# Kernel tuning notes

Measured on AMD Instinct MI355X. Metric: run time of the kernel, lower is better.

Reference implementation:

```python
import jax, jax.numpy as jnp
import numpy as np

D = 512
H = 8
DH = D // H
EPS = 1e-5


def layer_norm(x, gamma, beta):
    mu = jnp.mean(x, axis=-1, keepdims=True)
    var = jnp.mean(jnp.square(x - mu), axis=-1, keepdims=True)
    return (x - mu) * jax.lax.rsqrt(var + EPS) * gamma + beta


def setup_inputs() -> dict:
    key = jax.random.key(0)
    ks = jax.random.split(key, 16)
    B, N = 16, 1024
    s = 1.0 / np.sqrt(D)
    return {
        "h": jax.random.normal(ks[0], (B, N, D), jnp.float32),
        "ln1_g": jnp.ones((D,), jnp.float32),
        "ln1_b": jnp.zeros((D,), jnp.float32),
        "wq": jax.random.normal(ks[1], (D, D), jnp.float32) * s,
        "bq": jnp.zeros((D,), jnp.float32),
        "wk": jax.random.normal(ks[2], (D, D), jnp.float32) * s,
        "bk": jnp.zeros((D,), jnp.float32),
        "wv": jax.random.normal(ks[3], (D, D), jnp.float32) * s,
        "bv": jnp.zeros((D,), jnp.float32),
        "wo": jax.random.normal(ks[4], (D, D), jnp.float32) * s,
        "bo": jnp.zeros((D,), jnp.float32),
        "ln2_g": jnp.ones((D,), jnp.float32),
        "ln2_b": jnp.zeros((D,), jnp.float32),
        "w1": jax.random.normal(ks[5], (2 * D, D), jnp.float32) * s,
        "b1": jnp.zeros((2 * D,), jnp.float32),
        "w2": jax.random.normal(ks[6], (D, 2 * D), jnp.float32) * (1.0 / np.sqrt(2 * D)),
        "b2": jnp.zeros((D,), jnp.float32),
    }


def reference(h, ln1_g, ln1_b, wq, bq, wk, bk, wv, bv, wo, bo,
              ln2_g, ln2_b, w1, b1, w2, b2):
    B, N, _ = h.shape
    hn = layer_norm(h, ln1_g, ln1_b)
    # projections (torch Linear convention: x @ W^T + b)
    q = (hn @ wq.T + bq).reshape(B, N, H, DH)
    k = (hn @ wk.T + bk).reshape(B, N, H, DH)
    v = (hn @ wv.T + bv).reshape(B, N, H, DH)
    scores = jnp.einsum("bqhd,bkhd->bhqk", q, k) / np.sqrt(DH)
    attn = jax.nn.softmax(scores, axis=-1)  # [B,H,N,N]
    ctx = jnp.einsum("bhqk,bkhd->bqhd", attn, v).reshape(B, N, D)
    attn_out = ctx @ wo.T + bo
    # averaged attention weights (torch default average_attn_weights=True)
    attn_weights = jnp.mean(attn, axis=1)  # [B,N,N]
    h = h + attn_out
    # FFN: LN -> Linear(d,2d) -> SiLU -> Linear(2d,d), residual
    f = layer_norm(h, ln2_g, ln2_b)
    f = jax.nn.silu(f @ w1.T + b1) @ w2.T + b2
    h = h + f
    return h, attn_weights
```

## Files before the change

### kernel.cpp

```cpp
#include <hip/hip_runtime.h>

typedef unsigned short u16;
typedef __attribute__((ext_vector_type(8))) short short8;
typedef __attribute__((ext_vector_type(4))) float floatx4;
typedef __attribute__((ext_vector_type(16))) float floatx16;

#define MFMA_BF16(a, b, c) __builtin_amdgcn_mfma_f32_16x16x32_bf16((a), (b), (c), 0, 0, 0)
#define MFMA32(a, b, c) __builtin_amdgcn_mfma_f32_32x32x16_bf16((a), (b), (c), 0, 0, 0)

__device__ __forceinline__ u16 f2bf(float f) {
  unsigned b = __float_as_uint(f);
  b = b + 0x7FFFu + ((b >> 16) & 1u);
  return (u16)(b >> 16);
}

__device__ __forceinline__ float fexp8(float s) {
  float r;
  asm("v_exp_f32 %0, %1" : "=v"(r) : "v"(s * 0.18033688011112042f));
  return r;
}

__device__ __forceinline__ unsigned cvtpk(float a, float b) {
  unsigned r;
  asm("v_cvt_pk_bf16_f32 %0, %1, %2" : "=v"(r) : "v"(a), "v"(b));
  return r;
}

__device__ __forceinline__ void plswap(unsigned& x, unsigned& y) {
  asm("v_permlane32_swap_b32 %0, %1" : "+v"(x), "+v"(y));
}

__device__ __forceinline__ void gll16(const u16* g, u16* lds_uniform) {
  __builtin_amdgcn_global_load_lds(
      (const __attribute__((address_space(1))) void*)g,
      (__attribute__((address_space(3))) void*)lds_uniform, 16, 0, 0);
}

__global__ __launch_bounds__(256) void cast4_kernel(const float* __restrict__ src,
                                                    u16* __restrict__ dst, int n4) {
  int i = blockIdx.x * 256 + threadIdx.x;
  if (i < n4) {
    float4 v = ((const float4*)src)[i];
    ushort4 o;
    o.x = f2bf(v.x); o.y = f2bf(v.y); o.z = f2bf(v.z); o.w = f2bf(v.w);
    ((ushort4*)dst)[i] = o;
  }
}

__global__ __launch_bounds__(128) void ln_kernel(const float* __restrict__ x,
                                                 const float* __restrict__ g,
                                                 const float* __restrict__ be,
                                                 u16* __restrict__ y) {
  int row = blockIdx.x, t = threadIdx.x;
  float4 v = ((const float4*)(x + (size_t)row * 512))[t];
  float s = v.x + v.y + v.z + v.w;
  float q = v.x * v.x + v.y * v.y + v.z * v.z + v.w * v.w;
#pragma unroll
  for (int off = 32; off > 0; off >>= 1) {
    s += __shfl_xor(s, off);
    q += __shfl_xor(q, off);
  }
  __shared__ float sb[2], qb[2];
  int w = t >> 6;
  if ((t & 63) == 0) { sb[w] = s; qb[w] = q; }
  __syncthreads();
  s = sb[0] + sb[1];
  q = qb[0] + qb[1];
  float mu = s * (1.0f / 512.0f);
  float var = q * (1.0f / 512.0f) - mu * mu;
  float rs = rsqrtf(var + 1e-5f);
  float4 gg = ((const float4*)g)[t];
  float4 bb = ((const float4*)be)[t];
  ushort4 o;
  o.x = f2bf((v.x - mu) * rs * gg.x + bb.x);
  o.y = f2bf((v.y - mu) * rs * gg.y + bb.y);
  o.z = f2bf((v.z - mu) * rs * gg.z + bb.z);
  o.w = f2bf((v.w - mu) * rs * gg.w + bb.w);
  ((ushort4*)(y + (size_t)row * 512))[t] = o;
}

template <bool OUTB, bool SILU, bool RES>
__global__ __launch_bounds__(256) void gemm_bt_kernel(
    const u16* __restrict__ A, const u16* __restrict__ W,
    const float* __restrict__ bias, const float* __restrict__ res,
    void* __restrict__ out, int N, int K) {
  __shared__ __align__(16) u16 As[128 * 32];
  __shared__ __align__(16) u16 Bs[128 * 32];
  int t = threadIdx.x;
  int lane = t & 63, wave = t >> 6;
  int l15 = lane & 15, quad = lane >> 4;
  int rowBlk = blockIdx.y * 128, colBlk = blockIdx.x * 128;
  const u16* Ag = A + (size_t)(rowBlk + (t >> 2)) * K + (t & 3) * 8;
  const u16* Wg = W + (size_t)(colBlk + (t >> 2)) * K + (t & 3) * 8;
  u16* AsW = As + wave * 512;
  u16* BsW = Bs + wave * 512;
  int arow = (wave >> 1) * 64;
  int brow = (wave & 1) * 64;
  floatx4 acc[4][4] = {};
  for (int k0 = 0; k0 < K; k0 += 32) {
    gll16(Ag + k0, AsW);
    gll16(Ag + (size_t)64 * K + k0, AsW + 2048);
    gll16(Wg + k0, BsW);
    gll16(Wg + (size_t)64 * K + k0, BsW + 2048);
    __syncthreads();
    short8 a[4], b[4];
#pragma unroll
    for (int i = 0; i < 4; ++i)
      a[i] = *(const short8*)(As + (size_t)(arow + i * 16 + l15) * 32 + quad * 8);
#pragma unroll
    for (int j = 0; j < 4; ++j)
      b[j] = *(const short8*)(Bs + (size_t)(brow + j * 16 + l15) * 32 + quad * 8);
#pragma unroll
    for (int i = 0; i < 4; ++i)
#pragma unroll
      for (int j = 0; j < 4; ++j)
        acc[i][j] = MFMA_BF16(a[i], b[j], acc[i][j]);
    __syncthreads();
  }
#pragma unroll
  for (int j = 0; j < 4; ++j) {
    int col = colBlk + brow + j * 16 + l15;
    float bs = bias[col];
#pragma unroll
    for (int i = 0; i < 4; ++i) {
      int row0 = rowBlk + arow + i * 16 + quad * 4;
#pragma unroll
      for (int r = 0; r < 4; ++r) {
        size_t idx = (size_t)(row0 + r) * N + col;
        float v = acc[i][j][r] + bs;
        if (RES) v += res[idx];
        if (SILU) v = v * (1.0f / (1.0f + __expf(-v)));
        if (OUTB) ((u16*)out)[idx] = f2bf(v);
        else ((float*)out)[idx] = v;
      }
    }
  }
}

__global__ __launch_bounds__(256) void vtrans_kernel(const u16* __restrict__ qkv,
                                                     u16* __restrict__ vT) {
  __shared__ u16 tile[64][68];
  int blk = blockIdx.x;
  int b = blk >> 7, h = (blk >> 4) & 7, n0 = (blk & 15) * 64;
  int t = threadIdx.x;
#pragma unroll
  for (int rep = 0; rep < 16; ++rep) {
    int idx = t + rep * 256;
    int nl = idx >> 6, dh = idx & 63;
    tile[nl][dh] = qkv[(size_t)(b * 1024 + n0 + nl) * 1536 + 1024 + h * 64 + dh];
  }
  __syncthreads();
#pragma unroll
  for (int rep = 0; rep < 16; ++rep) {
    int idx = t + rep * 256;
    int dh = idx >> 6, nl = idx & 63;
    vT[((size_t)(b * 8 + h) * 64 + dh) * 1024 + n0 + nl] = tile[nl][dh];
  }
}

__global__ __launch_bounds__(256, 4) void attn_ctx_kernel(const u16* __restrict__ qkv,
                                                          const u16* __restrict__ vT,
                                                          u16* __restrict__ ctx,
                                                          float* __restrict__ linv_g) {
  __shared__ __align__(16) u16 Kb[2][4096];
  __shared__ __align__(16) u16 Vb[2][4096];
  int t = threadIdx.x, lane = t & 63, wave = t >> 6;
  int l31 = lane & 31, hi = lane >> 5;
  int bid = blockIdx.x;
  int L = (bid & 7) * 128 + (bid >> 3);
  int qblk = L & 7, h = (L >> 3) & 7, b = L >> 6;
  int q0w = qblk * 128 + wave * 32;

  short8 qf[4];
  const u16* qbase = qkv + (size_t)(b * 1024 + q0w + l31) * 1536 + h * 64;
#pragma unroll
  for (int t4 = 0; t4 < 4; ++t4)
    qf[t4] = *(const short8*)(qbase + t4 * 16 + hi * 8);

  short8 ones;
#pragma unroll
  for (int i = 0; i < 8; ++i) ones[i] = (short)0x3F80;

  floatx16 oacc[2] = {};
  floatx16 psum = {};

  const u16* krow = qkv + (size_t)(b * 1024 + lane) * 1536 + 512 + h * 64;
  const u16* vrow = vT + ((size_t)(b * 8 + h) * 64 + lane) * 1024;

  gll16(krow + wave * 8, &Kb[0][wave * 512]);
  gll16(krow + (wave + 4) * 8, &Kb[0][(wave + 4) * 512]);
  gll16(vrow + wave * 8, &Vb[0][wave * 512]);
  gll16(vrow + (wave + 4) * 8, &Vb[0][(wave + 4) * 512]);
  __syncthreads();

#pragma unroll 1
  for (int c = 0; c < 16; ++c) {
    int bf = c & 1;
    if (c < 15) {
      int nc = (c + 1) * 64;
      gll16(krow + (size_t)nc * 1536 + wave * 8, &Kb[bf ^ 1][wave * 512]);
      gll16(krow + (size_t)nc * 1536 + (wave + 4) * 8, &Kb[bf ^ 1][(wave + 4) * 512]);
      gll16(vrow + nc + wave * 8, &Vb[bf ^ 1][wave * 512]);
      gll16(vrow + nc + (wave + 4) * 8, &Vb[bf ^ 1][(wave + 4) * 512]);
    }
    short8 pa[4];
#pragma unroll
    for (int ct = 0; ct < 2; ++ct) {
      floatx16 s = {};
#pragma unroll
      for (int t4 = 0; t4 < 4; ++t4) {
        short8 kf = *(const short8*)&Kb[bf][(t4 * 2 + hi) * 512 + (ct * 32 + l31) * 8];
        s = MFMA32(kf, qf[t4], s);
      }
#pragma unroll
      for (int r = 0; r < 16; ++r) s[r] = fexp8(s[r]);
#pragma unroll
      for (int j = 0; j < 2; ++j) {
        unsigned a0 = cvtpk(s[j * 8 + 0], s[j * 8 + 1]);
        unsigned b0 = cvtpk(s[j * 8 + 4], s[j * 8 + 5]);
        unsigned a1 = cvtpk(s[j * 8 + 2], s[j * 8 + 3]);
        unsigned b1 = cvtpk(s[j * 8 + 6], s[j * 8 + 7]);
        plswap(a0, b0);
        plswap(a1, b1);
        union { unsigned u[4]; short8 v8; } uu;
        uu.u[0] = a0; uu.u[1] = a1; uu.u[2] = b0; uu.u[3] = b1;
        pa[ct * 2 + j] = uu.v8;
      }
    }
#pragma unroll
    for (int ks = 0; ks < 4; ++ks) {
      psum = MFMA32(pa[ks], ones, psum);
#pragma unroll
      for (int ct2 = 0; ct2 < 2; ++ct2) {
        short8 vf = *(const short8*)&Vb[bf][(ks * 2 + hi) * 512 + (ct2 * 32 + l31) * 8];
        oacc[ct2] = MFMA32(pa[ks], vf, oacc[ct2]);
      }
    }
    __syncthreads();
  }

  float il[16];
#pragma unroll
  for (int r = 0; r < 16; ++r) il[r] = 1.0f / psum[r];
  if (l31 == 0) {
#pragma unroll
    for (int reg = 0; reg < 16; ++reg) {
      int row = (reg & 3) + 8 * (reg >> 2) + 4 * hi;
      linv_g[(size_t)(b * 8 + h) * 1024 + q0w + row] = il[reg];
    }
  }
#pragma unroll
  for (int ct = 0; ct < 2; ++ct)
#pragma unroll
    for (int reg = 0; reg < 16; ++reg) {
      int row = (reg & 3) + 8 * (reg >> 2) + 4 * hi;
      ctx[(size_t)(b * 1024 + q0w + row) * 512 + h * 64 + ct * 32 + l31] =
          f2bf(oacc[ct][reg] * il[reg]);
    }
}

__global__ __launch_bounds__(256, 4) void attn_avg_kernel(const u16* __restrict__ qkv,
                                                          const float* __restrict__ linv_g,
                                                          float* __restrict__ attnw) {
  __shared__ __align__(16) u16 Kb[2][4096];
  int t = threadIdx.x, lane = t & 63, wave = t >> 6;
  int l31 = lane & 31, hi = lane >> 5;
  int bid = blockIdx.x;
  int L = (bid & 7) * 128 + (bid >> 3);
  int b = L >> 6;
  int r6 = L & 63;
  int kq = r6 & 7, qb = r6 >> 3;
  int q0w = qb * 128 + wave * 32;
  int key0 = kq * 128;

  const u16* qbase = qkv + (size_t)(b * 1024 + q0w + l31) * 1536;
  const u16* kbase0 = qkv + (size_t)(b * 1024 + key0 + lane) * 1536 + 512;

  gll16(kbase0 + wave * 8, &Kb[0][wave * 512]);
  gll16(kbase0 + (wave + 4) * 8, &Kb[0][(wave + 4) * 512]);
  __syncthreads();

  floatx16 avgacc[2] = {};
#pragma unroll 1
  for (int it = 0; it < 16; ++it) {
    int h = it & 7, chunk = it >> 3;
    int bf = it & 1;
    if (it < 15) {
      int nh = (it + 1) & 7, nc = (it + 1) >> 3;
      const u16* kb = kbase0 + (size_t)(nc * 64) * 1536 + nh * 64;
      gll16(kb + wave * 8, &Kb[bf ^ 1][wave * 512]);
      gll16(kb + (wave + 4) * 8, &Kb[bf ^ 1][(wave + 4) * 512]);
    }
    short8 qf[4];
#pragma unroll
    for (int t4 = 0; t4 < 4; ++t4)
      qf[t4] = *(const short8*)(qbase + h * 64 + t4 * 16 + hi * 8);
    const float* lg = linv_g + (size_t)(b * 8 + h) * 1024 + q0w + 4 * hi;
    float4 il0 = *(const float4*)(lg);
    float4 il1 = *(const float4*)(lg + 8);
    float4 il2 = *(const float4*)(lg + 16);
    float4 il3 = *(const float4*)(lg + 24);
    float il[16] = {il0.x, il0.y, il0.z, il0.w, il1.x, il1.y, il1.z, il1.w,
                    il2.x, il2.y, il2.z, il2.w, il3.x, il3.y, il3.z, il3.w};
    floatx16 sacc[2] = {};
#pragma unroll
    for (int ct = 0; ct < 2; ++ct)
#pragma unroll
      for (int t4 = 0; t4 < 4; ++t4) {
        short8 kf = *(const short8*)&Kb[bf][(t4 * 2 + hi) * 512 + (ct * 32 + l31) * 8];
        sacc[ct] = MFMA32(qf[t4], kf, sacc[ct]);
      }
#pragma unroll
    for (int ct = 0; ct < 2; ++ct)
#pragma unroll
      for (int r = 0; r < 16; ++r)
        avgacc[ct][r] += fexp8(sacc[ct][r]) * il[r];
    __syncthreads();
    if (h == 7) {
      int cb = key0 + chunk * 64;
#pragma unroll
      for (int ct = 0; ct < 2; ++ct)
#pragma unroll
        for (int r = 0; r < 16; ++r) {
          int row = (r & 3) + 8 * (r >> 2) + 4 * hi;
          __builtin_nontemporal_store(
              avgacc[ct][r] * 0.125f,
              &attnw[(size_t)(b * 1024 + q0w + row) * 1024 + cb + ct * 32 + l31]);
          avgacc[ct][r] = 0.f;
        }
    }
  }
}

extern "C" void kernel_launch(void* const* d_in, const int* in_sizes, int n_in,
                              void* d_out, int out_size, void* d_ws, size_t ws_size,
                              hipStream_t stream) {
  (void)in_sizes; (void)n_in; (void)out_size; (void)ws_size;
  const float* h   = (const float*)d_in[0];
  const float* g1  = (const float*)d_in[1];
  const float* be1 = (const float*)d_in[2];
  const float* wq  = (const float*)d_in[3];
  const float* bq  = (const float*)d_in[4];
  const float* wk  = (const float*)d_in[5];
  const float* bk  = (const float*)d_in[6];
  const float* wv  = (const float*)d_in[7];
  const float* bv  = (const float*)d_in[8];
  const float* wo  = (const float*)d_in[9];
  const float* bo  = (const float*)d_in[10];
  const float* g2  = (const float*)d_in[11];
  const float* be2 = (const float*)d_in[12];
  const float* w1  = (const float*)d_in[13];
  const float* b1  = (const float*)d_in[14];
  const float* w2  = (const float*)d_in[15];
  const float* b2  = (const float*)d_in[16];

  char* p = (char*)d_ws;
  auto carve = [&](size_t bytes) {
    char* r = p;
    p += (bytes + 255) & ~(size_t)255;
    return r;
  };
  u16*   wcat = (u16*)carve((size_t)1536 * 512 * 2);
  u16*   wob  = (u16*)carve((size_t)512 * 512 * 2);
  u16*   w1b  = (u16*)carve((size_t)1024 * 512 * 2);
  u16*   w2b  = (u16*)carve((size_t)512 * 1024 * 2);
  float* bcat = (float*)carve((size_t)1536 * 4);
  u16*   hn   = (u16*)carve((size_t)16384 * 512 * 2);
  u16*   qkvb = (u16*)carve((size_t)16384 * 1536 * 2);
  u16*   vTb  = (u16*)carve((size_t)16384 * 512 * 2);
  u16*   ctxb = (u16*)carve((size_t)16384 * 512 * 2);
  u16*   fb   = (u16*)carve((size_t)16384 * 512 * 2);
  u16*   gb   = (u16*)carve((size_t)16384 * 1024 * 2);
  float* linv = (float*)carve((size_t)16 * 8 * 1024 * 4);

  float* outh = (float*)d_out;
  float* outattn = outh + (size_t)16384 * 512;

  cast4_kernel<<<256, 256, 0, stream>>>(wq, wcat, 65536);
  cast4_kernel<<<256, 256, 0, stream>>>(wk, wcat + 512 * 512, 65536);
  cast4_kernel<<<256, 256, 0, stream>>>(wv, wcat + 2 * 512 * 512, 65536);
  cast4_kernel<<<256, 256, 0, stream>>>(wo, wob, 65536);
  cast4_kernel<<<512, 256, 0, stream>>>(w1, w1b, 131072);
  cast4_kernel<<<512, 256, 0, stream>>>(w2, w2b, 131072);
  hipMemcpyAsync(bcat, bq, 512 * 4, hipMemcpyDeviceToDevice, stream);
  hipMemcpyAsync(bcat + 512, bk, 512 * 4, hipMemcpyDeviceToDevice, stream);
  hipMemcpyAsync(bcat + 1024, bv, 512 * 4, hipMemcpyDeviceToDevice, stream);

  ln_kernel<<<16384, 128, 0, stream>>>(h, g1, be1, hn);
  gemm_bt_kernel<true, false, false><<<dim3(12, 128), 256, 0, stream>>>(
      hn, wcat, bcat, nullptr, qkvb, 1536, 512);
  vtrans_kernel<<<2048, 256, 0, stream>>>(qkvb, vTb);
  attn_ctx_kernel<<<1024, 256, 0, stream>>>(qkvb, vTb, ctxb, linv);
  attn_avg_kernel<<<1024, 256, 0, stream>>>(qkvb, linv, outattn);
  gemm_bt_kernel<false, false, true><<<dim3(4, 128), 256, 0, stream>>>(
      ctxb, wob, bo, h, outh, 512, 512);
  ln_kernel<<<16384, 128, 0, stream>>>(outh, g2, be2, fb);
  gemm_bt_kernel<true, true, false><<<dim3(8, 128), 256, 0, stream>>>(
      fb, w1b, b1, nullptr, gb, 1024, 512);
  gemm_bt_kernel<false, false, true><<<dim3(4, 128), 256, 0, stream>>>(
      gb, w2b, b2, outh, outh, 512, 1024);
}
```

Measured before the change: 439.9 us.

## Triple-buffer K tiles in attention-average kernel with explicit vmcnt waits

Moves the attention-weight averaging kernel from double to triple buffering of K tiles in shared memory, prefetching two iterations ahead. A full __syncthreads is replaced by a raw s_barrier preceded by targeted s_waitcnt vmcnt counts, so the nontemporal output stores do not have to drain before the next iteration. This is meant to hide global-load latency and cut barrier stalls, at the cost of 50% more LDS per block (which could lower occupancy) and fragile hand-tuned vmcnt counts that depend on how many memory ops the compiler emits.

```diff
diff --git a/kernel.cpp b/kernel.cpp
--- a/kernel.cpp
+++ b/kernel.cpp
@@ -262,7 +262,7 @@
 __global__ __launch_bounds__(256, 4) void attn_avg_kernel(const u16* __restrict__ qkv,
                                                           const float* __restrict__ linv_g,
                                                           float* __restrict__ attnw) {
-  __shared__ __align__(16) u16 Kb[2][4096];
+  __shared__ __align__(16) u16 Kb[3][4096];
   int t = threadIdx.x, lane = t & 63, wave = t >> 6;
   int l31 = lane & 31, hi = lane >> 5;
   int bid = blockIdx.x;
@@ -276,21 +276,26 @@
   const u16* qbase = qkv + (size_t)(b * 1024 + q0w + l31) * 1536;
   const u16* kbase0 = qkv + (size_t)(b * 1024 + key0 + lane) * 1536 + 512;
 
-  gll16(kbase0 + wave * 8, &Kb[0][wave * 512]);
-  gll16(kbase0 + (wave + 4) * 8, &Kb[0][(wave + 4) * 512]);
-  __syncthreads();
+  u16* bufA = &Kb[0][0];
+  u16* bufB = &Kb[1][0];
+  u16* bufC = &Kb[2][0];
+
+  auto stage = [&](int it, u16* buf) {
+    int sh = it & 7, sc = it >> 3;
+    const u16* kb = kbase0 + (size_t)(sc * 64) * 1536 + sh * 64;
+    gll16(kb + wave * 8, buf + wave * 512);
+    gll16(kb + (wave + 4) * 8, buf + (wave + 4) * 512);
+  };
+
+  stage(0, bufA);
+  stage(1, bufB);
+  asm volatile("s_waitcnt vmcnt(2)" ::: "memory");
+  __builtin_amdgcn_s_barrier();
 
   floatx16 avgacc[2] = {};
 #pragma unroll 1
   for (int it = 0; it < 16; ++it) {
     int h = it & 7, chunk = it >> 3;
-    int bf = it & 1;
-    if (it < 15) {
-      int nh = (it + 1) & 7, nc = (it + 1) >> 3;
-      const u16* kb = kbase0 + (size_t)(nc * 64) * 1536 + nh * 64;
-      gll16(kb + wave * 8, &Kb[bf ^ 1][wave * 512]);
-      gll16(kb + (wave + 4) * 8, &Kb[bf ^ 1][(wave + 4) * 512]);
-    }
     short8 qf[4];
 #pragma unroll
     for (int t4 = 0; t4 < 4; ++t4)
@@ -302,12 +307,16 @@
     float4 il3 = *(const float4*)(lg + 24);
     float il[16] = {il0.x, il0.y, il0.z, il0.w, il1.x, il1.y, il1.z, il1.w,
                     il2.x, il2.y, il2.z, il2.w, il3.x, il3.y, il3.z, il3.w};
+    asm volatile("" ::: "memory");
+    int pf = (it + 2 < 16) ? it + 2 : 15;
+    stage(pf, bufC);
+    asm volatile("" ::: "memory");
     floatx16 sacc[2] = {};
 #pragma unroll
     for (int ct = 0; ct < 2; ++ct)
 #pragma unroll
       for (int t4 = 0; t4 < 4; ++t4) {
-        short8 kf = *(const short8*)&Kb[bf][(t4 * 2 + hi) * 512 + (ct * 32 + l31) * 8];
+        short8 kf = *(const short8*)(bufA + (t4 * 2 + hi) * 512 + (ct * 32 + l31) * 8);
         sacc[ct] = MFMA32(qf[t4], kf, sacc[ct]);
       }
 #pragma unroll
@@ -315,7 +324,6 @@
 #pragma unroll
       for (int r = 0; r < 16; ++r)
         avgacc[ct][r] += fexp8(sacc[ct][r]) * il[r];
-    __syncthreads();
     if (h == 7) {
       int cb = key0 + chunk * 64;
 #pragma unroll
@@ -328,7 +336,12 @@
               &attnw[(size_t)(b * 1024 + q0w + row) * 1024 + cb + ct * 32 + l31]);
           avgacc[ct][r] = 0.f;
         }
-    }
+      asm volatile("s_waitcnt vmcnt(34)" ::: "memory");
+    } else {
+      asm volatile("s_waitcnt vmcnt(2)" ::: "memory");
+    }
+    __builtin_amdgcn_s_barrier();
+    u16* tmp = bufA; bufA = bufB; bufB = bufC; bufC = tmp;
   }
 }
 
```

New measurement: 451.1 us. +2.6%, slower.
